# Optimization experiments

Hardware: AMD Instinct MI355X
Metric: run time of the kernel (lower is better)

Reference implementation:

```python
import jax, jax.numpy as jnp
import numpy as np

SCALE = 16 / 8  # alpha / r

def setup_inputs() -> dict:
    key = jax.random.key(0)
    k1, k2, k3 = jax.random.split(key, 3)
    x = jax.random.normal(k1, (4, 2048, 4096), dtype=jnp.float32)
    A = jax.random.normal(k2, (4096, 8), dtype=jnp.float32)
    B = jax.random.normal(k3, (8, 4096), dtype=jnp.float32)
    return {"x": x, "A": A, "B": B}

def reference(x, A, B):
    # Faithful to torch module: materialize W = A @ B * scale, then x @ W
    W = (A @ B) * SCALE            # [dim, dim_out]
    return x @ W                   # [b, s, dim_out]
```

## Files before the change

kernel.cpp:

```cpp
#include <hip/hip_runtime.h>


#define DIM    4096
#define DIM4   (DIM / 4)
#define RANK   8
#define LORA_SCALE 2.0f
#define BLOCK  256
#define CHUNK  4
#define RPB    4

__global__ __launch_bounds__(BLOCK) void transpose_A_kernel(
    const float* __restrict__ A, float* __restrict__ At)
{
    const int o = blockIdx.x * BLOCK + threadIdx.x;
    const int r = o >> 12;
    const int i = o & (DIM - 1);
    At[o] = A[(size_t)i * RANK + r];
}

__global__ __launch_bounds__(BLOCK) void lora_fused_kernel(
    const float* __restrict__ x,
    const float* __restrict__ At,
    const float* __restrict__ B,
    float* __restrict__ out)
{
    const int tid  = threadIdx.x;
    const int row0 = blockIdx.x * RPB;
    const float4* x4  = (const float4*)x;
    const float4* At4 = (const float4*)At;
    const float4* B4  = (const float4*)B;
    float4* out4 = (float4*)out;

    float acc[RPB][RANK];
#pragma unroll
    for (int m = 0; m < RPB; ++m)
#pragma unroll
        for (int r = 0; r < RANK; ++r) acc[m][r] = 0.0f;

#pragma unroll
    for (int k = 0; k < CHUNK; ++k) {
        const int i4 = tid + BLOCK * k;
        float4 a[RANK];
#pragma unroll
        for (int r = 0; r < RANK; ++r) a[r] = At4[r * DIM4 + i4];
#pragma unroll
        for (int m = 0; m < RPB; ++m) {
            const float4 xv = x4[(size_t)(row0 + m) * DIM4 + i4];
#pragma unroll
            for (int r = 0; r < RANK; ++r) {
                acc[m][r] += xv.x * a[r].x + xv.y * a[r].y
                           + xv.z * a[r].z + xv.w * a[r].w;
            }
        }
    }

#pragma unroll
    for (int m = 0; m < RPB; ++m)
#pragma unroll
        for (int r = 0; r < RANK; ++r)
#pragma unroll
            for (int off = 32; off > 0; off >>= 1)
                acc[m][r] += __shfl_down(acc[m][r], off, 64);

    __shared__ float red[BLOCK / 64][RPB][RANK];
    __shared__ float tf[RPB][RANK];
    const int wave = tid >> 6;
    const int lane = tid & 63;
    if (lane == 0) {
#pragma unroll
        for (int m = 0; m < RPB; ++m)
#pragma unroll
            for (int r = 0; r < RANK; ++r) red[wave][m][r] = acc[m][r];
    }
    __syncthreads();
    if (tid < RPB * RANK) {
        const int m = tid / RANK;
        const int r = tid % RANK;
        tf[m][r] = (red[0][m][r] + red[1][m][r] + red[2][m][r] + red[3][m][r])
                   * LORA_SCALE;
    }
    __syncthreads();

    float tv[RPB][RANK];
#pragma unroll
    for (int m = 0; m < RPB; ++m)
#pragma unroll
        for (int r = 0; r < RANK; ++r) tv[m][r] = tf[m][r];

#pragma unroll
    for (int k = 0; k < CHUNK; ++k) {
        const int i4 = tid + BLOCK * k;
        float4 b[RANK];
#pragma unroll
        for (int r = 0; r < RANK; ++r) b[r] = B4[r * DIM4 + i4];
#pragma unroll
        for (int m = 0; m < RPB; ++m) {
            float4 o = make_float4(0.f, 0.f, 0.f, 0.f);
#pragma unroll
            for (int r = 0; r < RANK; ++r) {
                o.x += tv[m][r] * b[r].x;
                o.y += tv[m][r] * b[r].y;
                o.z += tv[m][r] * b[r].z;
                o.w += tv[m][r] * b[r].w;
            }
            out4[(size_t)(row0 + m) * DIM4 + i4] = o;
        }
    }
}

extern "C" void kernel_launch(void* const* d_in, const int* in_sizes, int n_in,
                              void* d_out, int out_size, void* d_ws, size_t ws_size,
                              hipStream_t stream) {
    const float* x = (const float*)d_in[0];
    const float* A = (const float*)d_in[1];
    const float* B = (const float*)d_in[2];
    float* out = (float*)d_out;
    float* At  = (float*)d_ws;

    const int rows = in_sizes[0] / DIM;

    transpose_A_kernel<<<(RANK * DIM) / BLOCK, BLOCK, 0, stream>>>(A, At);
    lora_fused_kernel<<<rows / RPB, BLOCK, 0, stream>>>(x, At, B, out);
}
```

Before: 242.3 us.

## Assign rows per wavefront, read A directly, and use nontemporal output stores

Each wavefront now owns two full rows and handles the whole reduction with xor-shuffles. This removes the shared-memory cross-wave reduction and both block barriers. The separate A-transpose kernel launch is dropped: A is read in its native layout as eight float4 per input element group. Output is written with nontemporal stores to avoid polluting the cache, and launch bounds add an occupancy hint. In exchange, each wave loops over the full dimension serially, and A/B are re-read per wave rather than shared across rows.

```diff
diff --git a/kernel.cpp b/kernel.cpp
--- a/kernel.cpp
+++ b/kernel.cpp
@@ -6,104 +6,98 @@
 #define RANK   8
 #define LORA_SCALE 2.0f
 #define BLOCK  256
-#define CHUNK  4
-#define RPB    4
+#define WPB    4
+#define ROWS   2
+#define RPB    (WPB * ROWS)
+#define ITERS  (DIM4 / 64)
 
-__global__ __launch_bounds__(BLOCK) void transpose_A_kernel(
-    const float* __restrict__ A, float* __restrict__ At)
+typedef float f32x4 __attribute__((ext_vector_type(4)));
+
+__device__ __forceinline__ void fma8(float acc[RANK], float xe,
+                                     const float4& lo, const float4& hi)
 {
-    const int o = blockIdx.x * BLOCK + threadIdx.x;
-    const int r = o >> 12;
-    const int i = o & (DIM - 1);
-    At[o] = A[(size_t)i * RANK + r];
+    acc[0] += xe * lo.x; acc[1] += xe * lo.y;
+    acc[2] += xe * lo.z; acc[3] += xe * lo.w;
+    acc[4] += xe * hi.x; acc[5] += xe * hi.y;
+    acc[6] += xe * hi.z; acc[7] += xe * hi.w;
 }
 
-__global__ __launch_bounds__(BLOCK) void lora_fused_kernel(
+__global__ __launch_bounds__(BLOCK, 4) void lora_fused_kernel(
     const float* __restrict__ x,
-    const float* __restrict__ At,
+    const float* __restrict__ A,
     const float* __restrict__ B,
     float* __restrict__ out)
 {
     const int tid  = threadIdx.x;
-    const int row0 = blockIdx.x * RPB;
-    const float4* x4  = (const float4*)x;
-    const float4* At4 = (const float4*)At;
-    const float4* B4  = (const float4*)B;
-    float4* out4 = (float4*)out;
+    const int wave = tid >> 6;
+    const int lane = tid & 63;
+    const size_t row0 = (size_t)blockIdx.x * RPB + (size_t)wave * ROWS;
 
-    float acc[RPB][RANK];
+    const float4* __restrict__ x4  = (const float4*)x;
+    const float4* __restrict__ A4  = (const float4*)A;
+    const float4* __restrict__ B4  = (const float4*)B;
+    f32x4* __restrict__ out4 = (f32x4*)out;
+
+    float acc[ROWS][RANK];
 #pragma unroll
-    for (int m = 0; m < RPB; ++m)
+    for (int m = 0; m < ROWS; ++m)
 #pragma unroll
         for (int r = 0; r < RANK; ++r) acc[m][r] = 0.0f;
 
+#pragma unroll 2
+    for (int k = 0; k < ITERS; ++k) {
+        const int i4 = lane + 64 * k;
+        float4 xa[ROWS];
 #pragma unroll
-    for (int k = 0; k < CHUNK; ++k) {
-        const int i4 = tid + BLOCK * k;
-        float4 a[RANK];
+        for (int m = 0; m < ROWS; ++m)
+            xa[m] = x4[(row0 + m) * DIM4 + i4];
+        float4 a[8];
 #pragma unroll
-        for (int r = 0; r < RANK; ++r) a[r] = At4[r * DIM4 + i4];
+        for (int j = 0; j < 8; ++j)
+            a[j] = A4[8 * i4 + j];
 #pragma unroll
-        for (int m = 0; m < RPB; ++m) {
-            const float4 xv = x4[(size_t)(row0 + m) * DIM4 + i4];
-#pragma unroll
-            for (int r = 0; r < RANK; ++r) {
-                acc[m][r] += xv.x * a[r].x + xv.y * a[r].y
-                           + xv.z * a[r].z + xv.w * a[r].w;
-            }
+        for (int m = 0; m < ROWS; ++m) {
+            fma8(acc[m], xa[m].x, a[0], a[1]);
+            fma8(acc[m], xa[m].y, a[2], a[3]);
+            fma8(acc[m], xa[m].z, a[4], a[5]);
+            fma8(acc[m], xa[m].w, a[6], a[7]);
         }
     }
 
+    float t[ROWS][RANK];
 #pragma unroll
-    for (int m = 0; m < RPB; ++m)
+    for (int m = 0; m < ROWS; ++m)
+#pragma unroll
+        for (int r = 0; r < RANK; ++r) {
+            float v = acc[m][r];
+#pragma unroll
+            for (int off = 1; off < 64; off <<= 1)
+                v += __shfl_xor(v, off, 64);
+            t[m][r] = v * LORA_SCALE;
+        }
+
+#pragma unroll 2
+    for (int k = 0; k < ITERS; ++k) {
+        const int i4 = lane + 64 * k;
+        float4 b[RANK];
 #pragma unroll
         for (int r = 0; r < RANK; ++r)
+            b[r] = B4[(size_t)r * DIM4 + i4];
 #pragma unroll
-            for (int off = 32; off > 0; off >>= 1)
-                acc[m][r] += __shfl_down(acc[m][r], off, 64);
-
-    __shared__ float red[BLOCK / 64][RPB][RANK];
-    __shared__ float tf[RPB][RANK];
-    const int wave = tid >> 6;
-    const int lane = tid & 63;
-    if (lane == 0) {
+        for (int m = 0; m < ROWS; ++m) {
+            float4 o;
+            o.x = t[m][0] * b[0].x; o.y = t[m][0] * b[0].y;
+            o.z = t[m][0] * b[0].z; o.w = t[m][0] * b[0].w;
 #pragma unroll
-        for (int m = 0; m < RPB; ++m)
-#pragma unroll
-            for (int r = 0; r < RANK; ++r) red[wave][m][r] = acc[m][r];
-    }
-    __syncthreads();
-    if (tid < RPB * RANK) {
-        const int m = tid / RANK;
-        const int r = tid % RANK;
-        tf[m][r] = (red[0][m][r] + red[1][m][r] + red[2][m][r] + red[3][m][r])
-                   * LORA_SCALE;
-    }
-    __syncthreads();
-
-    float tv[RPB][RANK];
-#pragma unroll
-    for (int m = 0; m < RPB; ++m)
-#pragma unroll
-        for (int r = 0; r < RANK; ++r) tv[m][r] = tf[m][r];
-
-#pragma unroll
-    for (int k = 0; k < CHUNK; ++k) {
-        const int i4 = tid + BLOCK * k;
-        float4 b[RANK];
-#pragma unroll
-        for (int r = 0; r < RANK; ++r) b[r] = B4[r * DIM4 + i4];
-#pragma unroll
-        for (int m = 0; m < RPB; ++m) {
-            float4 o = make_float4(0.f, 0.f, 0.f, 0.f);
-#pragma unroll
-            for (int r = 0; r < RANK; ++r) {
-                o.x += tv[m][r] * b[r].x;
-                o.y += tv[m][r] * b[r].y;
-                o.z += tv[m][r] * b[r].z;
-                o.w += tv[m][r] * b[r].w;
+            for (int r = 1; r < RANK; ++r) {
+                o.x += t[m][r] * b[r].x;
+                o.y += t[m][r] * b[r].y;
+                o.z += t[m][r] * b[r].z;
+                o.w += t[m][r] * b[r].w;
             }
-            out4[(size_t)(row0 + m) * DIM4 + i4] = o;
+            f32x4 ov;
+            ov.x = o.x; ov.y = o.y; ov.z = o.z; ov.w = o.w;
+            __builtin_nontemporal_store(ov, &out4[(row0 + m) * DIM4 + i4]);
         }
     }
 }
@@ -115,10 +109,8 @@
     const float* A = (const float*)d_in[1];
     const float* B = (const float*)d_in[2];
     float* out = (float*)d_out;
-    float* At  = (float*)d_ws;
 
     const int rows = in_sizes[0] / DIM;
 
-    transpose_A_kernel<<<(RANK * DIM) / BLOCK, BLOCK, 0, stream>>>(A, At);
-    lora_fused_kernel<<<rows / RPB, BLOCK, 0, stream>>>(x, At, B, out);
+    lora_fused_kernel<<<rows / RPB, BLOCK, 0, stream>>>(x, A, B, out);
 }
```

Result: slower. 306.2 us (+26.4%).
